# Performance work log

Hardware: AMD Instinct MI355X
Metric: run time of the kernel (lower is better)

## Reference

```python
import jax, jax.numpy as jnp
import numpy as np

N, C, B, HF, WF, HID = 200000, 128, 4, 116, 200, 64
STRIDE = 8
MAX_BEV_RANGE = 72.0
LN_EPS = 1e-5


def setup_inputs() -> dict:
    key = jax.random.key(0)
    ks = jax.random.split(key, 20)
    s = 0.05  # weight scale
    x = jax.random.normal(ks[0], (N, C), jnp.float32)
    # sparse voxel indices: (batch, z, y, x) on a 128x128x5 stride-8 grid
    bi = jax.random.randint(ks[1], (N, 1), 0, B)
    zi = jax.random.randint(ks[2], (N, 1), 0, 5)
    yi = jax.random.randint(ks[3], (N, 1), 0, 128)
    xi = jax.random.randint(ks[4], (N, 1), 0, 128)
    indices = jnp.concatenate([bi, zi, yi, xi], axis=1).astype(jnp.int32)
    voxel_size = jnp.array([0.1, 0.1, 0.2], jnp.float32)
    pc_range = jnp.array([-51.2, -51.2, -5.0, 51.2, 51.2, 3.0], jnp.float32)
    # plausible lidar->image projection: cam_x=-y, cam_y=-z, cam_z=x, K=[1000,800;1000,450]
    Rt = np.array([[0.0, -1.0, 0.0, 0.0],
                   [0.0, 0.0, -1.0, 1.6],
                   [1.0, 0.0, 0.0, 0.0]], np.float32)
    K = np.array([[1000.0, 0.0, 800.0], [0.0, 1000.0, 450.0], [0.0, 0.0, 1.0]], np.float32)
    P = K @ Rt  # [3,4]
    trans = jnp.asarray(np.tile(P[None], (B, 1, 1)))
    trans = trans + 0.01 * jax.random.normal(ks[5], (B, 3, 4), jnp.float32)
    img_feats = jax.random.normal(ks[6], (B, C, HF, WF), jnp.float32)
    return {
        'x': x, 'indices': indices, 'voxel_size': voxel_size, 'pc_range': pc_range,
        'trans_lidar_to_img': trans, 'img_feats': img_feats, 'img_h': 928, 'img_w': 1600,
        'fg_w1': s * jax.random.normal(ks[7], (C, HID)), 'fg_b1': jnp.zeros((HID,)),
        'fg_w2': s * jax.random.normal(ks[8], (HID, 1)), 'fg_b2': jnp.zeros((1,)),
        'rt_w1': s * jax.random.normal(ks[9], (C + 3, HID)), 'rt_b1': jnp.zeros((HID,)),
        'rt_w2': s * jax.random.normal(ks[10], (HID, 3)),
        'rt_b2': jnp.array([2.0, 0.0, -1.0], jnp.float32),
        'le_w1': s * jax.random.normal(ks[11], (2 * C, C)), 'le_b1': jnp.zeros((C,)),
        'le_w2': s * jax.random.normal(ks[12], (C, C)), 'le_b2': jnp.zeros((C,)),
        'ln_g': jnp.ones((C,)), 'ln_b': jnp.zeros((C,)),
    }


def _bilinear_sample(img_t, b, u_norm, v_norm):
    # img_t: [B,H,W,C]; grid_sample bilinear, align_corners=True, padding_mode='zeros'
    Hf, Wf = img_t.shape[1], img_t.shape[2]
    px = (u_norm + 1.0) * 0.5 * (Wf - 1)
    py = (v_norm + 1.0) * 0.5 * (Hf - 1)
    x0 = jnp.floor(px)
    y0 = jnp.floor(py)
    fx, fy = px - x0, py - y0
    x0i, y0i = x0.astype(jnp.int32), y0.astype(jnp.int32)
    out = jnp.zeros((px.shape[0], img_t.shape[-1]), img_t.dtype)
    for dy in (0, 1):
        for dx in (0, 1):
            xi, yi = x0i + dx, y0i + dy
            w = (fx if dx else 1.0 - fx) * (fy if dy else 1.0 - fy)
            inb = (xi >= 0) & (xi < Wf) & (yi >= 0) & (yi < Hf)
            f = img_t[b, jnp.clip(yi, 0, Hf - 1), jnp.clip(xi, 0, Wf - 1)]
            out = out + f * (w * inb.astype(w.dtype))[:, None]
    return out


def _layernorm(h, g, b):
    mu = jnp.mean(h, axis=-1, keepdims=True)
    var = jnp.mean(jnp.square(h - mu), axis=-1, keepdims=True)
    return (h - mu) * jax.lax.rsqrt(var + LN_EPS) * g + b


def reference(x, indices, voxel_size, pc_range, trans_lidar_to_img, img_feats,
              img_h, img_w, fg_w1, fg_b1, fg_w2, fg_b2, rt_w1, rt_b1, rt_w2, rt_b2,
              le_w1, le_b1, le_w2, le_b2, ln_g, ln_b):
    # voxel centers: indices[:,1:]=(z,y,x) -> (x,y,z)
    spatial = indices[:, 1:][:, ::-1].astype(jnp.float32)
    cvs = voxel_size * STRIDE
    centers = spatial * cvs + pc_range[:3] + cvs / 2.0  # [N,3]
    range_norm = jnp.linalg.norm(centers[:, :2], axis=-1, keepdims=True)
    range_norm = jnp.clip(range_norm / max(MAX_BEV_RANGE, 1e-6), 0.0, 1.0)

    # project to image plane
    ones = jnp.ones((centers.shape[0], 1), centers.dtype)
    xyz_hom = jnp.concatenate([centers, ones], axis=1)  # [N,4]
    batch_ids = indices[:, 0]
    P = trans_lidar_to_img[batch_ids]  # [N,3,4]
    pts = jnp.einsum('nij,nj->ni', P, xyz_hom)
    depth = pts[:, 2]
    safe = jnp.maximum(depth, 1e-5)
    u_feat = pts[:, 0] / safe * (float(WF) / float(img_w))
    v_feat = pts[:, 1] / safe * (float(HF) / float(img_h))
    u_norm = 2.0 * (u_feat / max(WF - 1, 1)) - 1.0
    v_norm = 2.0 * (v_feat / max(HF - 1, 1)) - 1.0
    valid = (depth > 1e-5) & (jnp.abs(u_norm) <= 1.0) & (jnp.abs(v_norm) <= 1.0)
    valid_f = valid.astype(jnp.float32)[:, None]  # [N,1]

    # router
    p_fg = jax.nn.sigmoid(jax.nn.relu(x @ fg_w1 + fg_b1) @ fg_w2 + fg_b2)  # [N,1]
    rin = jnp.concatenate([x, range_norm, p_fg, valid_f], axis=-1)
    route_weights = jax.nn.softmax(jax.nn.relu(rin @ rt_w1 + rt_b1) @ rt_w2 + rt_b2, axis=-1)

    # per-point grid_sample gather from image features
    img_t = jnp.transpose(img_feats, (0, 2, 3, 1))  # [B,H,W,C]
    sampled = _bilinear_sample(img_t, batch_ids, u_norm, v_norm)  # [N,C]

    # light fusion expert
    h = jnp.concatenate([x, sampled], axis=-1)
    delta_light = (jax.nn.relu(h @ le_w1 + le_b1) @ le_w2 + le_b2) * valid_f
    delta = route_weights[:, 1:2] * delta_light  # rectified expert disabled (RECTIFY_RATIO=0)

    fusion_gain = jnp.linalg.norm(delta, axis=-1, keepdims=True) / (
        jnp.linalg.norm(x, axis=-1, keepdims=True) + 1e-6)
    fusion_gain = jnp.clip(1.0 - jnp.exp(-fusion_gain), 0.0, 1.0)

    fused = _layernorm(x + delta, ln_g, ln_b)  # [N,C]

    zeros1 = jnp.zeros_like(p_fg)
    quality = jnp.clip(jnp.concatenate(
        [route_weights, p_fg, range_norm, valid_f, zeros1, fusion_gain,
         zeros1, zeros1, zeros1], axis=-1), 0.0, 1.0)  # [N,11]
    return fused, quality
```

## Files before the change

kernel.cpp:

```cpp
#include <hip/hip_runtime.h>

namespace {

typedef __attribute__((ext_vector_type(8))) short bf16x8;
typedef __attribute__((ext_vector_type(4))) float f32x4;

constexpr int C     = 128;
constexpr int HF    = 116;
constexpr int WF    = 200;
constexpr int PTILE = 32;
constexpr int BLK   = 256;
constexpr int NPTS  = 200000;
constexpr int AS_STRIDE  = 264;
constexpr int HID_STRIDE = 136;

constexpr int W_LE1 = 0;
constexpr int W_LE2 = 32768;
constexpr int W_FG  = 49152;
constexpr int W_RT  = 57344;
constexpr size_t IMG_BYTE_OFF = 131072;

constexpr int IMG_BLOCKS = 4 * HF * 2;
constexpr int WP_BLOCKS  = 256;

__device__ __forceinline__ float b2f(unsigned short u) {
  union { unsigned int i; float f; } v; v.i = ((unsigned int)u) << 16; return v.f;
}
__device__ __forceinline__ unsigned short f2b(float f) {
  union { float f; unsigned int i; } v; v.f = f;
  unsigned int i = v.i;
  return (unsigned short)((i + 0x7fffu + ((i >> 16) & 1u)) >> 16);
}
__device__ __forceinline__ void unp(unsigned int u, float& lo, float& hi) {
  union { unsigned int i; float f; } a, b;
  a.i = u << 16; b.i = u & 0xffff0000u; lo = a.f; hi = b.f;
}
__device__ __forceinline__ unsigned int packb(float a, float b) {
  unsigned int r;
  asm("v_cvt_pk_bf16_f32 %0, %1, %2" : "=v"(r) : "v"(a), "v"(b));
  return r;
}

__global__ __launch_bounds__(BLK) void prep_kernel(
    const float* __restrict__ imgf,
    const float* __restrict__ le_w1, const float* __restrict__ le_w2,
    const float* __restrict__ fg_w1, const float* __restrict__ rt_w1,
    short* __restrict__ wpack, short* __restrict__ imgT) {
  __shared__ short buf[100 * HID_STRIDE];
  const int blk = blockIdx.x;
  if (blk < IMG_BLOCKS) {
    const int half = blk & 1, by = blk >> 1;
    const int b = by / HF, y = by - b * HF;
    const int x0 = half * 100;
    const float* s = imgf + (size_t)b * C * HF * WF + (size_t)y * WF + x0;
    for (int i = threadIdx.x; i < C * 25; i += BLK) {
      int c = i / 25, qx = i - c * 25;
      float4 v = *(const float4*)(s + (size_t)c * (HF * WF) + qx * 4);
      int xb = qx * 4;
      buf[(xb + 0) * HID_STRIDE + c] = (short)f2b(v.x);
      buf[(xb + 1) * HID_STRIDE + c] = (short)f2b(v.y);
      buf[(xb + 2) * HID_STRIDE + c] = (short)f2b(v.z);
      buf[(xb + 3) * HID_STRIDE + c] = (short)f2b(v.w);
    }
    __syncthreads();
    short* d = imgT + ((size_t)(b * HF + y) * WF + x0) * C;
    for (int i = threadIdx.x; i < 100 * 16; i += BLK) {
      int xx = i >> 4, c8 = (i & 15) << 3;
      *(uint4*)(d + (size_t)xx * C + c8) = *(const uint4*)&buf[xx * HID_STRIDE + c8];
    }
  } else {
    int idx = (blk - IMG_BLOCKS) * BLK + threadIdx.x;
    if (idx < 32768) {
      int k = idx >> 7, n = idx & 127;
      wpack[W_LE1 + (((k >> 3) * 128 + n) << 3) + (k & 7)] = (short)f2b(le_w1[idx]);
    } else if (idx < 49152) {
      int l = idx - 32768; int k = l >> 7, n = l & 127;
      wpack[W_LE2 + (((k >> 3) * 128 + n) << 3) + (k & 7)] = (short)f2b(le_w2[l]);
    } else if (idx < 57344) {
      int l = idx - 49152; int k = l >> 6, n = l & 63;
      wpack[W_FG + (((k >> 3) * 64 + n) << 3) + (k & 7)] = (short)f2b(fg_w1[l]);
    } else {
      int l = idx - 57344; int k = l >> 6, n = l & 63;
      wpack[W_RT + (((k >> 3) * 64 + n) << 3) + (k & 7)] = (short)f2b(rt_w1[k * 64 + n]);
    }
  }
}

__global__ __launch_bounds__(BLK, 6) void fuse_kernel(
    const float* __restrict__ x,
    const int*   __restrict__ indices,
    const float* __restrict__ vox, const float* __restrict__ pcr,
    const float* __restrict__ trans,
    const int* __restrict__ imgh_p, const int* __restrict__ imgw_p,
    const float* __restrict__ fg_b1v, const float* __restrict__ fg_w2v,
    const float* __restrict__ fg_b2v,
    const float* __restrict__ rt_w1f,
    const float* __restrict__ rt_b1v, const float* __restrict__ rt_w2v,
    const float* __restrict__ rt_b2v,
    const float* __restrict__ le_b1v, const float* __restrict__ le_b2v,
    const float* __restrict__ ln_gv, const float* __restrict__ ln_bv,
    const short* __restrict__ wpack,
    const short* __restrict__ imgT,
    float* __restrict__ out_fused, float* __restrict__ out_qual) {
  __shared__ short As[PTILE * AS_STRIDE];
  __shared__ float s_rn[32], s_pfg[32], s_valid[32], s_px[32], s_py[32];
  __shared__ float s_gain[32], s_rv[32];
  __shared__ float s_route[32][3];
  __shared__ int   s_bat[32];
  __shared__ __align__(16) float s_lnpart[4][16][4];

  const int tid  = threadIdx.x;
  const int n0   = blockIdx.x * PTILE;
  const int wave = tid >> 6;
  const int lane = tid & 63;
  const int q    = lane >> 4;
  const int nn   = lane & 15;

  {
    const float4* xsrc = (const float4*)(x + (size_t)n0 * C);
    for (int i = tid; i < PTILE * C / 4; i += BLK) {
      float4 v = xsrc[i];
      int p = i >> 5, c4 = (i & 31) * 4;
      uint2 sv = { packb(v.x, v.y), packb(v.z, v.w) };
      *(uint2*)&As[p * AS_STRIDE + c4] = sv;
    }
  }
  if (tid < PTILE) {
    int p = tid;
    int base = (n0 + p) * 4;
    int bi = indices[base + 0], zi = indices[base + 1];
    int yi = indices[base + 2], xi = indices[base + 3];
    float sp[3] = { (float)xi, (float)yi, (float)zi };
    float cen[3];
#pragma unroll
    for (int k = 0; k < 3; ++k) {
      float cvs = vox[k] * 8.0f;
      cen[k] = sp[k] * cvs + pcr[k] + cvs * 0.5f;
    }
    float rn = sqrtf(cen[0] * cen[0] + cen[1] * cen[1]) / 72.0f;
    rn = fminf(fmaxf(rn, 0.0f), 1.0f);
    float pt[3];
#pragma unroll
    for (int r = 0; r < 3; ++r) {
      const float* row = trans + (bi * 3 + r) * 4;
      pt[r] = row[0] * cen[0] + row[1] * cen[1] + row[2] * cen[2] + row[3];
    }
    float depth = pt[2];
    float safe  = fmaxf(depth, 1e-5f);
    float uf = pt[0] / safe * ((float)WF / (float)imgw_p[0]);
    float vf = pt[1] / safe * ((float)HF / (float)imgh_p[0]);
    float un = 2.0f * (uf / (float)(WF - 1)) - 1.0f;
    float vn = 2.0f * (vf / (float)(HF - 1)) - 1.0f;
    bool valid = (depth > 1e-5f) && (fabsf(un) <= 1.0f) && (fabsf(vn) <= 1.0f);
    s_rn[p] = rn;
    s_valid[p] = valid ? 1.0f : 0.0f;
    s_bat[p] = bi;
    s_px[p] = (un + 1.0f) * 0.5f * (float)(WF - 1);
    s_py[p] = (vn + 1.0f) * 0.5f * (float)(HF - 1);
  }
  __syncthreads();

  f32x4 accS[4];
#pragma unroll
  for (int t = 0; t < 4; ++t) accS[t] = (f32x4){0.f, 0.f, 0.f, 0.f};
  if (wave < 2) {
    const int p0 = wave * 16;
    const bf16x8* Bfg = (const bf16x8*)(wpack + W_FG);
#pragma unroll 2
    for (int ks = 0; ks < 4; ++ks) {
      bf16x8 a = *(const bf16x8*)&As[(p0 + nn) * AS_STRIDE + ks * 32 + q * 8];
#pragma unroll
      for (int t = 0; t < 4; ++t) {
        bf16x8 b = Bfg[(ks * 4 + q) * 64 + t * 16 + nn];
        accS[t] = __builtin_amdgcn_mfma_f32_16x16x32_bf16(a, b, accS[t], 0, 0, 0);
      }
    }
    float part[4] = {0.f, 0.f, 0.f, 0.f};
#pragma unroll
    for (int t = 0; t < 4; ++t) {
      int col = t * 16 + nn;
      float bias = fg_b1v[col];
      float wv2  = fg_w2v[col];
#pragma unroll
      for (int r = 0; r < 4; ++r)
        part[r] += fmaxf(accS[t][r] + bias, 0.f) * wv2;
    }
#pragma unroll
    for (int off = 1; off < 16; off <<= 1) {
#pragma unroll
      for (int r = 0; r < 4; ++r) part[r] += __shfl_xor(part[r], off);
    }
    if (nn == 0) {
      float b2 = fg_b2v[0];
#pragma unroll
      for (int r = 0; r < 4; ++r)
        s_pfg[p0 + q * 4 + r] = 1.f / (1.f + expf(-(part[r] + b2)));
    }
  } else {
    const int p0 = (wave - 2) * 16;
    const bf16x8* Brt = (const bf16x8*)(wpack + W_RT);
#pragma unroll 2
    for (int ks = 0; ks < 4; ++ks) {
      bf16x8 a = *(const bf16x8*)&As[(p0 + nn) * AS_STRIDE + ks * 32 + q * 8];
#pragma unroll
      for (int t = 0; t < 4; ++t) {
        bf16x8 b = Brt[(ks * 4 + q) * 64 + t * 16 + nn];
        accS[t] = __builtin_amdgcn_mfma_f32_16x16x32_bf16(a, b, accS[t], 0, 0, 0);
      }
    }
  }
  __syncthreads();

  if (wave >= 2) {
    const int p0 = (wave - 2) * 16;
    float lg0[4] = {0,0,0,0}, lg1[4] = {0,0,0,0}, lg2[4] = {0,0,0,0};
#pragma unroll
    for (int t = 0; t < 4; ++t) {
      int col = t * 16 + nn;
      float b1 = rt_b1v[col];
      float wr = rt_w1f[128 * 64 + col];
      float wp = rt_w1f[129 * 64 + col];
      float wv = rt_w1f[130 * 64 + col];
      float w20 = rt_w2v[col * 3 + 0], w21 = rt_w2v[col * 3 + 1], w22 = rt_w2v[col * 3 + 2];
#pragma unroll
      for (int r = 0; r < 4; ++r) {
        int p = p0 + q * 4 + r;
        float h = accS[t][r] + b1 + s_rn[p] * wr + s_pfg[p] * wp + s_valid[p] * wv;
        h = fmaxf(h, 0.f);
        lg0[r] += h * w20; lg1[r] += h * w21; lg2[r] += h * w22;
      }
    }
#pragma unroll
    for (int off = 1; off < 16; off <<= 1) {
#pragma unroll
      for (int r = 0; r < 4; ++r) {
        lg0[r] += __shfl_xor(lg0[r], off);
        lg1[r] += __shfl_xor(lg1[r], off);
        lg2[r] += __shfl_xor(lg2[r], off);
      }
    }
    if (nn == 0) {
      float rb0 = rt_b2v[0], rb1 = rt_b2v[1], rb2 = rt_b2v[2];
#pragma unroll
      for (int r = 0; r < 4; ++r) {
        int p = p0 + q * 4 + r;
        float l0 = lg0[r] + rb0, l1 = lg1[r] + rb1, l2 = lg2[r] + rb2;
        float m = fmaxf(l0, fmaxf(l1, l2));
        float e0 = expf(l0 - m), e1 = expf(l1 - m), e2 = expf(l2 - m);
        float inv = 1.f / (e0 + e1 + e2);
        s_route[p][0] = e0 * inv; s_route[p][1] = e1 * inv; s_route[p][2] = e2 * inv;
        s_rv[p] = e1 * inv * s_valid[p];
      }
    }
  }
  {
    int p = tid >> 3, grp = tid & 7, ch0 = grp * 16;
    float sacc[16];
#pragma unroll
    for (int k = 0; k < 16; ++k) sacc[k] = 0.f;
    if (s_valid[p] > 0.5f) {
      float px = s_px[p], py = s_py[p];
      float x0f = floorf(px), y0f = floorf(py);
      float fx = px - x0f, fy = py - y0f;
      int ix = (int)x0f, iy = (int)y0f;
      int bb = s_bat[p];
#pragma unroll
      for (int dy = 0; dy < 2; ++dy) {
#pragma unroll
        for (int dx = 0; dx < 2; ++dx) {
          int xi = ix + dx, yi = iy + dy;
          if (xi >= 0 && xi < WF && yi >= 0 && yi < HF) {
            float w = (dx ? fx : 1.0f - fx) * (dy ? fy : 1.0f - fy);
            const short* tp = imgT + (((size_t)bb * HF + yi) * WF + xi) * C + ch0;
            uint4 u0 = *(const uint4*)tp;
            uint4 u1 = *(const uint4*)(tp + 8);
            float lo, hi;
            unp(u0.x, lo, hi); sacc[0] += w * lo;  sacc[1] += w * hi;
            unp(u0.y, lo, hi); sacc[2] += w * lo;  sacc[3] += w * hi;
            unp(u0.z, lo, hi); sacc[4] += w * lo;  sacc[5] += w * hi;
            unp(u0.w, lo, hi); sacc[6] += w * lo;  sacc[7] += w * hi;
            unp(u1.x, lo, hi); sacc[8] += w * lo;  sacc[9] += w * hi;
            unp(u1.y, lo, hi); sacc[10] += w * lo; sacc[11] += w * hi;
            unp(u1.z, lo, hi); sacc[12] += w * lo; sacc[13] += w * hi;
            unp(u1.w, lo, hi); sacc[14] += w * lo; sacc[15] += w * hi;
          }
        }
      }
    }
    uint4 o0 = { packb(sacc[0], sacc[1]),  packb(sacc[2], sacc[3]),
                 packb(sacc[4], sacc[5]),  packb(sacc[6], sacc[7]) };
    uint4 o1 = { packb(sacc[8], sacc[9]),  packb(sacc[10], sacc[11]),
                 packb(sacc[12], sacc[13]), packb(sacc[14], sacc[15]) };
    *(uint4*)&As[p * AS_STRIDE + 128 + ch0]     = o0;
    *(uint4*)&As[p * AS_STRIDE + 128 + ch0 + 8] = o1;
  }
  __syncthreads();

  const int pt = wave & 1, cg = wave >> 1;
  const int p0le = pt * 16;
  const bf16x8* Ble1 = (const bf16x8*)(wpack + W_LE1);
  f32x4 acc[4];
#pragma unroll
  for (int t = 0; t < 4; ++t) acc[t] = (f32x4){0.f, 0.f, 0.f, 0.f};
#pragma unroll 2
  for (int ks = 0; ks < 8; ++ks) {
    bf16x8 a = *(const bf16x8*)&As[(p0le + nn) * AS_STRIDE + ks * 32 + q * 8];
#pragma unroll
    for (int t = 0; t < 4; ++t) {
      bf16x8 b = Ble1[(ks * 4 + q) * 128 + (cg * 4 + t) * 16 + nn];
      acc[t] = __builtin_amdgcn_mfma_f32_16x16x32_bf16(a, b, acc[t], 0, 0, 0);
    }
  }
  __syncthreads();
#pragma unroll
  for (int t = 0; t < 4; ++t) {
    int col = (cg * 4 + t) * 16 + nn;
    float bias = le_b1v[col];
#pragma unroll
    for (int r = 0; r < 4; ++r)
      As[(p0le + q * 4 + r) * AS_STRIDE + 128 + col] =
          (short)f2b(fmaxf(acc[t][r] + bias, 0.f));
  }
  __syncthreads();

  const bf16x8* Ble2 = (const bf16x8*)(wpack + W_LE2);
  f32x4 acc2[4];
#pragma unroll
  for (int t = 0; t < 4; ++t) acc2[t] = (f32x4){0.f, 0.f, 0.f, 0.f};
#pragma unroll 2
  for (int ks = 0; ks < 4; ++ks) {
    bf16x8 a = *(const bf16x8*)&As[(p0le + nn) * AS_STRIDE + 128 + ks * 32 + q * 8];
#pragma unroll
    for (int t = 0; t < 4; ++t) {
      bf16x8 b = Ble2[(ks * 4 + q) * 128 + (cg * 4 + t) * 16 + nn];
      acc2[t] = __builtin_amdgcn_mfma_f32_16x16x32_bf16(a, b, acc2[t], 0, 0, 0);
    }
  }
  float yv[4][4];
  float psum[4] = {0,0,0,0}, psum2[4] = {0,0,0,0}, pd2[4] = {0,0,0,0}, px2[4] = {0,0,0,0};
#pragma unroll
  for (int t = 0; t < 4; ++t) {
    int col = (cg * 4 + t) * 16 + nn;
    float bias = le_b2v[col];
#pragma unroll
    for (int r = 0; r < 4; ++r) {
      int p = p0le + q * 4 + r;
      float d  = (acc2[t][r] + bias) * s_rv[p];
      float xv = b2f((unsigned short)As[p * AS_STRIDE + col]);
      float y  = xv + d;
      yv[t][r] = y;
      psum[r]  += y;       psum2[r] += y * y;
      pd2[r]   += d * d;   px2[r]   += xv * xv;
    }
  }
#pragma unroll
  for (int off = 1; off < 16; off <<= 1) {
#pragma unroll
    for (int r = 0; r < 4; ++r) {
      psum[r]  += __shfl_xor(psum[r], off);
      psum2[r] += __shfl_xor(psum2[r], off);
      pd2[r]   += __shfl_xor(pd2[r], off);
      px2[r]   += __shfl_xor(px2[r], off);
    }
  }
  if (nn == 0) {
#pragma unroll
    for (int r = 0; r < 4; ++r) {
      f32x4 st = { psum[r], psum2[r], pd2[r], px2[r] };
      *(f32x4*)&s_lnpart[wave][q * 4 + r][0] = st;
    }
  }
  __syncthreads();
  {
    float gcol[4], bcol[4];
#pragma unroll
    for (int t = 0; t < 4; ++t) {
      int col = (cg * 4 + t) * 16 + nn;
      gcol[t] = ln_gv[col]; bcol[t] = ln_bv[col];
    }
#pragma unroll
    for (int r = 0; r < 4; ++r) {
      int lr = q * 4 + r;
      int p  = p0le + lr;
      f32x4 oth = *(const f32x4*)&s_lnpart[wave ^ 2][lr][0];
      float sy  = psum[r]  + oth[0];
      float sy2 = psum2[r] + oth[1];
      float sd2 = pd2[r]   + oth[2];
      float sx2 = px2[r]   + oth[3];
      float mu  = sy * (1.f / 128.f);
      float var = sy2 * (1.f / 128.f) - mu * mu;
      float inv = rsqrtf(var + 1e-5f);
      if (wave < 2 && nn == 0) {
        float gain = sqrtf(sd2) / (sqrtf(sx2) + 1e-6f);
        s_gain[p] = fminf(fmaxf(1.f - expf(-gain), 0.f), 1.f);
      }
      float* orow = out_fused + (size_t)(n0 + p) * C;
#pragma unroll
      for (int t = 0; t < 4; ++t) {
        int col = (cg * 4 + t) * 16 + nn;
        orow[col] = (yv[t][r] - mu) * inv * gcol[t] + bcol[t];
      }
    }
  }
  __syncthreads();

  for (int idx = tid; idx < PTILE * 11; idx += BLK) {
    int p2 = idx / 11, k = idx - p2 * 11;
    float v = 0.0f;
    if (k < 3)       v = s_route[p2][k];
    else if (k == 3) v = s_pfg[p2];
    else if (k == 4) v = s_rn[p2];
    else if (k == 5) v = s_valid[p2];
    else if (k == 7) v = s_gain[p2];
    v = fminf(fmaxf(v, 0.0f), 1.0f);
    out_qual[(size_t)(n0 + p2) * 11 + k] = v;
  }
}

}

extern "C" void kernel_launch(void* const* d_in, const int* in_sizes, int n_in,
                              void* d_out, int out_size, void* d_ws, size_t ws_size,
                              hipStream_t stream) {
  const float* x       = (const float*)d_in[0];
  const int*   indices = (const int*)d_in[1];
  const float* vox     = (const float*)d_in[2];
  const float* pcr     = (const float*)d_in[3];
  const float* trans   = (const float*)d_in[4];
  const float* imgf    = (const float*)d_in[5];
  const int*   imgh    = (const int*)d_in[6];
  const int*   imgw    = (const int*)d_in[7];
  const float* fg_w1   = (const float*)d_in[8];
  const float* fg_b1   = (const float*)d_in[9];
  const float* fg_w2   = (const float*)d_in[10];
  const float* fg_b2   = (const float*)d_in[11];
  const float* rt_w1   = (const float*)d_in[12];
  const float* rt_b1   = (const float*)d_in[13];
  const float* rt_w2   = (const float*)d_in[14];
  const float* rt_b2   = (const float*)d_in[15];
  const float* le_w1   = (const float*)d_in[16];
  const float* le_b1   = (const float*)d_in[17];
  const float* le_w2   = (const float*)d_in[18];
  const float* le_b2   = (const float*)d_in[19];
  const float* ln_g    = (const float*)d_in[20];
  const float* ln_b    = (const float*)d_in[21];

  short* wpack = (short*)d_ws;
  short* imgT  = (short*)((char*)d_ws + IMG_BYTE_OFF);

  float* out_fused = (float*)d_out;
  float* out_qual  = out_fused + (size_t)NPTS * C;

  (void)in_sizes; (void)n_in; (void)out_size; (void)ws_size;

  prep_kernel<<<IMG_BLOCKS + WP_BLOCKS, BLK, 0, stream>>>(
      imgf, le_w1, le_w2, fg_w1, rt_w1, wpack, imgT);
  fuse_kernel<<<NPTS / PTILE, BLK, 0, stream>>>(
      x, indices, vox, pcr, trans, imgh, imgw,
      fg_b1, fg_w2, fg_b2,
      rt_w1, rt_b1, rt_w2, rt_b2,
      le_b1, le_b2, ln_g, ln_b,
      wpack, imgT, out_fused, out_qual);
}
```

Before: 339.7 us.

## Double point tile to 64 and reuse weight fragments across row groups

Raises the per-block point tile from 32 to 64 and restructures the small MLP and light-expert GEMMs so each wave loads B weight fragments once and applies them to several 16-row groups. The first light-expert layer is repartitioned so each wave owns two output column tiles across all 64 rows, and the second layer plus layernorm loop runs over two halves. This is meant to cut redundant global weight loads per point and halve the block count, at the cost of more registers and LDS per block (launch bound lowered to 4 blocks per CU) and extra barriers in the second-layer loop.

```diff
diff --git a/kernel.cpp b/kernel.cpp
--- a/kernel.cpp
+++ b/kernel.cpp
@@ -8,7 +8,7 @@
 constexpr int C     = 128;
 constexpr int HF    = 116;
 constexpr int WF    = 200;
-constexpr int PTILE = 32;
+constexpr int PTILE = 64;
 constexpr int BLK   = 256;
 constexpr int NPTS  = 200000;
 constexpr int AS_STRIDE  = 264;
@@ -86,7 +86,7 @@
   }
 }
 
-__global__ __launch_bounds__(BLK, 6) void fuse_kernel(
+__global__ __launch_bounds__(BLK, 4) void fuse_kernel(
     const float* __restrict__ x,
     const int*   __restrict__ indices,
     const float* __restrict__ vox, const float* __restrict__ pcr,
@@ -103,10 +103,10 @@
     const short* __restrict__ imgT,
     float* __restrict__ out_fused, float* __restrict__ out_qual) {
   __shared__ short As[PTILE * AS_STRIDE];
-  __shared__ float s_rn[32], s_pfg[32], s_valid[32], s_px[32], s_py[32];
-  __shared__ float s_gain[32], s_rv[32];
-  __shared__ float s_route[32][3];
-  __shared__ int   s_bat[32];
+  __shared__ float s_rn[64], s_pfg[64], s_valid[64], s_px[64], s_py[64];
+  __shared__ float s_gain[64], s_rv[64];
+  __shared__ float s_route[64][3];
+  __shared__ int   s_bat[64];
   __shared__ __align__(16) float s_lnpart[4][16][4];
 
   const int tid  = threadIdx.x;
@@ -139,16 +139,16 @@
     }
     float rn = sqrtf(cen[0] * cen[0] + cen[1] * cen[1]) / 72.0f;
     rn = fminf(fmaxf(rn, 0.0f), 1.0f);
-    float pt[3];
+    float pt3[3];
 #pragma unroll
     for (int r = 0; r < 3; ++r) {
       const float* row = trans + (bi * 3 + r) * 4;
-      pt[r] = row[0] * cen[0] + row[1] * cen[1] + row[2] * cen[2] + row[3];
-    }
-    float depth = pt[2];
+      pt3[r] = row[0] * cen[0] + row[1] * cen[1] + row[2] * cen[2] + row[3];
+    }
+    float depth = pt3[2];
     float safe  = fmaxf(depth, 1e-5f);
-    float uf = pt[0] / safe * ((float)WF / (float)imgw_p[0]);
-    float vf = pt[1] / safe * ((float)HF / (float)imgh_p[0]);
+    float uf = pt3[0] / safe * ((float)WF / (float)imgw_p[0]);
+    float vf = pt3[1] / safe * ((float)HF / (float)imgh_p[0]);
     float un = 2.0f * (uf / (float)(WF - 1)) - 1.0f;
     float vn = 2.0f * (vf / (float)(HF - 1)) - 1.0f;
     bool valid = (depth > 1e-5f) && (fabsf(un) <= 1.0f) && (fabsf(vn) <= 1.0f);
@@ -160,60 +160,64 @@
   }
   __syncthreads();
 
-  f32x4 accS[4];
-#pragma unroll
-  for (int t = 0; t < 4; ++t) accS[t] = (f32x4){0.f, 0.f, 0.f, 0.f};
+  const int p032 = (wave & 1) * 32;
+  f32x4 accS[4][2];
+#pragma unroll
+  for (int t = 0; t < 4; ++t)
+#pragma unroll
+    for (int rg = 0; rg < 2; ++rg) accS[t][rg] = (f32x4){0.f, 0.f, 0.f, 0.f};
+  {
+    const bf16x8* Bw = (const bf16x8*)(wpack + (wave < 2 ? W_FG : W_RT));
+    for (int ks = 0; ks < 4; ++ks) {
+      bf16x8 b0 = Bw[(ks * 4 + q) * 64 + 0 * 16 + nn];
+      bf16x8 b1 = Bw[(ks * 4 + q) * 64 + 1 * 16 + nn];
+      bf16x8 b2 = Bw[(ks * 4 + q) * 64 + 2 * 16 + nn];
+      bf16x8 b3 = Bw[(ks * 4 + q) * 64 + 3 * 16 + nn];
+#pragma unroll
+      for (int rg = 0; rg < 2; ++rg) {
+        bf16x8 a = *(const bf16x8*)&As[(p032 + rg * 16 + nn) * AS_STRIDE + ks * 32 + q * 8];
+        accS[0][rg] = __builtin_amdgcn_mfma_f32_16x16x32_bf16(a, b0, accS[0][rg], 0, 0, 0);
+        accS[1][rg] = __builtin_amdgcn_mfma_f32_16x16x32_bf16(a, b1, accS[1][rg], 0, 0, 0);
+        accS[2][rg] = __builtin_amdgcn_mfma_f32_16x16x32_bf16(a, b2, accS[2][rg], 0, 0, 0);
+        accS[3][rg] = __builtin_amdgcn_mfma_f32_16x16x32_bf16(a, b3, accS[3][rg], 0, 0, 0);
+      }
+    }
+  }
   if (wave < 2) {
-    const int p0 = wave * 16;
-    const bf16x8* Bfg = (const bf16x8*)(wpack + W_FG);
-#pragma unroll 2
-    for (int ks = 0; ks < 4; ++ks) {
-      bf16x8 a = *(const bf16x8*)&As[(p0 + nn) * AS_STRIDE + ks * 32 + q * 8];
-#pragma unroll
-      for (int t = 0; t < 4; ++t) {
-        bf16x8 b = Bfg[(ks * 4 + q) * 64 + t * 16 + nn];
-        accS[t] = __builtin_amdgcn_mfma_f32_16x16x32_bf16(a, b, accS[t], 0, 0, 0);
-      }
-    }
-    float part[4] = {0.f, 0.f, 0.f, 0.f};
+    float part[2][4] = {{0.f,0.f,0.f,0.f},{0.f,0.f,0.f,0.f}};
 #pragma unroll
     for (int t = 0; t < 4; ++t) {
       int col = t * 16 + nn;
       float bias = fg_b1v[col];
       float wv2  = fg_w2v[col];
 #pragma unroll
-      for (int r = 0; r < 4; ++r)
-        part[r] += fmaxf(accS[t][r] + bias, 0.f) * wv2;
+      for (int rg = 0; rg < 2; ++rg)
+#pragma unroll
+        for (int r = 0; r < 4; ++r)
+          part[rg][r] += fmaxf(accS[t][rg][r] + bias, 0.f) * wv2;
     }
 #pragma unroll
     for (int off = 1; off < 16; off <<= 1) {
 #pragma unroll
-      for (int r = 0; r < 4; ++r) part[r] += __shfl_xor(part[r], off);
+      for (int rg = 0; rg < 2; ++rg)
+#pragma unroll
+        for (int r = 0; r < 4; ++r) part[rg][r] += __shfl_xor(part[rg][r], off);
     }
     if (nn == 0) {
-      float b2 = fg_b2v[0];
-#pragma unroll
-      for (int r = 0; r < 4; ++r)
-        s_pfg[p0 + q * 4 + r] = 1.f / (1.f + expf(-(part[r] + b2)));
-    }
-  } else {
-    const int p0 = (wave - 2) * 16;
-    const bf16x8* Brt = (const bf16x8*)(wpack + W_RT);
-#pragma unroll 2
-    for (int ks = 0; ks < 4; ++ks) {
-      bf16x8 a = *(const bf16x8*)&As[(p0 + nn) * AS_STRIDE + ks * 32 + q * 8];
-#pragma unroll
-      for (int t = 0; t < 4; ++t) {
-        bf16x8 b = Brt[(ks * 4 + q) * 64 + t * 16 + nn];
-        accS[t] = __builtin_amdgcn_mfma_f32_16x16x32_bf16(a, b, accS[t], 0, 0, 0);
-      }
+      float b2s = fg_b2v[0];
+#pragma unroll
+      for (int rg = 0; rg < 2; ++rg)
+#pragma unroll
+        for (int r = 0; r < 4; ++r)
+          s_pfg[p032 + rg * 16 + q * 4 + r] = 1.f / (1.f + expf(-(part[rg][r] + b2s)));
     }
   }
   __syncthreads();
 
   if (wave >= 2) {
-    const int p0 = (wave - 2) * 16;
-    float lg0[4] = {0,0,0,0}, lg1[4] = {0,0,0,0}, lg2[4] = {0,0,0,0};
+    float lg0[2][4] = {{0,0,0,0},{0,0,0,0}};
+    float lg1[2][4] = {{0,0,0,0},{0,0,0,0}};
+    float lg2[2][4] = {{0,0,0,0},{0,0,0,0}};
 #pragma unroll
     for (int t = 0; t < 4; ++t) {
       int col = t * 16 + nn;
@@ -223,38 +227,44 @@
       float wv = rt_w1f[130 * 64 + col];
       float w20 = rt_w2v[col * 3 + 0], w21 = rt_w2v[col * 3 + 1], w22 = rt_w2v[col * 3 + 2];
 #pragma unroll
-      for (int r = 0; r < 4; ++r) {
-        int p = p0 + q * 4 + r;
-        float h = accS[t][r] + b1 + s_rn[p] * wr + s_pfg[p] * wp + s_valid[p] * wv;
-        h = fmaxf(h, 0.f);
-        lg0[r] += h * w20; lg1[r] += h * w21; lg2[r] += h * w22;
-      }
+      for (int rg = 0; rg < 2; ++rg)
+#pragma unroll
+        for (int r = 0; r < 4; ++r) {
+          int p = p032 + rg * 16 + q * 4 + r;
+          float h = accS[t][rg][r] + b1 + s_rn[p] * wr + s_pfg[p] * wp + s_valid[p] * wv;
+          h = fmaxf(h, 0.f);
+          lg0[rg][r] += h * w20; lg1[rg][r] += h * w21; lg2[rg][r] += h * w22;
+        }
     }
 #pragma unroll
     for (int off = 1; off < 16; off <<= 1) {
 #pragma unroll
-      for (int r = 0; r < 4; ++r) {
-        lg0[r] += __shfl_xor(lg0[r], off);
-        lg1[r] += __shfl_xor(lg1[r], off);
-        lg2[r] += __shfl_xor(lg2[r], off);
-      }
+      for (int rg = 0; rg < 2; ++rg)
+#pragma unroll
+        for (int r = 0; r < 4; ++r) {
+          lg0[rg][r] += __shfl_xor(lg0[rg][r], off);
+          lg1[rg][r] += __shfl_xor(lg1[rg][r], off);
+          lg2[rg][r] += __shfl_xor(lg2[rg][r], off);
+        }
     }
     if (nn == 0) {
       float rb0 = rt_b2v[0], rb1 = rt_b2v[1], rb2 = rt_b2v[2];
 #pragma unroll
-      for (int r = 0; r < 4; ++r) {
-        int p = p0 + q * 4 + r;
-        float l0 = lg0[r] + rb0, l1 = lg1[r] + rb1, l2 = lg2[r] + rb2;
-        float m = fmaxf(l0, fmaxf(l1, l2));
-        float e0 = expf(l0 - m), e1 = expf(l1 - m), e2 = expf(l2 - m);
-        float inv = 1.f / (e0 + e1 + e2);
-        s_route[p][0] = e0 * inv; s_route[p][1] = e1 * inv; s_route[p][2] = e2 * inv;
-        s_rv[p] = e1 * inv * s_valid[p];
-      }
-    }
-  }
-  {
-    int p = tid >> 3, grp = tid & 7, ch0 = grp * 16;
+      for (int rg = 0; rg < 2; ++rg)
+#pragma unroll
+        for (int r = 0; r < 4; ++r) {
+          int p = p032 + rg * 16 + q * 4 + r;
+          float l0 = lg0[rg][r] + rb0, l1 = lg1[rg][r] + rb1, l2 = lg2[rg][r] + rb2;
+          float m = fmaxf(l0, fmaxf(l1, l2));
+          float e0 = expf(l0 - m), e1 = expf(l1 - m), e2 = expf(l2 - m);
+          float inv = 1.f / (e0 + e1 + e2);
+          s_route[p][0] = e0 * inv; s_route[p][1] = e1 * inv; s_route[p][2] = e2 * inv;
+          s_rv[p] = e1 * inv * s_valid[p];
+        }
+    }
+  }
+  for (int it = 0; it < 2; ++it) {
+    int p = it * 32 + (tid >> 3), grp = tid & 7, ch0 = grp * 16;
     float sacc[16];
 #pragma unroll
     for (int k = 0; k < 16; ++k) sacc[k] = 0.f;
@@ -296,113 +306,121 @@
   }
   __syncthreads();
 
+  {
+    const bf16x8* Ble1 = (const bf16x8*)(wpack + W_LE1);
+    f32x4 acc[2][4];
+#pragma unroll
+    for (int t2 = 0; t2 < 2; ++t2)
+#pragma unroll
+      for (int rg = 0; rg < 4; ++rg) acc[t2][rg] = (f32x4){0.f, 0.f, 0.f, 0.f};
+    for (int ks = 0; ks < 8; ++ks) {
+      bf16x8 b0 = Ble1[(ks * 4 + q) * 128 + (wave * 2 + 0) * 16 + nn];
+      bf16x8 b1 = Ble1[(ks * 4 + q) * 128 + (wave * 2 + 1) * 16 + nn];
+#pragma unroll
+      for (int rg = 0; rg < 4; ++rg) {
+        bf16x8 a = *(const bf16x8*)&As[(rg * 16 + nn) * AS_STRIDE + ks * 32 + q * 8];
+        acc[0][rg] = __builtin_amdgcn_mfma_f32_16x16x32_bf16(a, b0, acc[0][rg], 0, 0, 0);
+        acc[1][rg] = __builtin_amdgcn_mfma_f32_16x16x32_bf16(a, b1, acc[1][rg], 0, 0, 0);
+      }
+    }
+    __syncthreads();
+#pragma unroll
+    for (int t2 = 0; t2 < 2; ++t2) {
+      int col = (wave * 2 + t2) * 16 + nn;
+      float bias = le_b1v[col];
+#pragma unroll
+      for (int rg = 0; rg < 4; ++rg)
+#pragma unroll
+        for (int r = 0; r < 4; ++r)
+          As[(rg * 16 + q * 4 + r) * AS_STRIDE + 128 + col] =
+              (short)f2b(fmaxf(acc[t2][rg][r] + bias, 0.f));
+    }
+    __syncthreads();
+  }
+
+  const bf16x8* Ble2 = (const bf16x8*)(wpack + W_LE2);
   const int pt = wave & 1, cg = wave >> 1;
-  const int p0le = pt * 16;
-  const bf16x8* Ble1 = (const bf16x8*)(wpack + W_LE1);
-  f32x4 acc[4];
-#pragma unroll
-  for (int t = 0; t < 4; ++t) acc[t] = (f32x4){0.f, 0.f, 0.f, 0.f};
-#pragma unroll 2
-  for (int ks = 0; ks < 8; ++ks) {
-    bf16x8 a = *(const bf16x8*)&As[(p0le + nn) * AS_STRIDE + ks * 32 + q * 8];
-#pragma unroll
-    for (int t = 0; t < 4; ++t) {
-      bf16x8 b = Ble1[(ks * 4 + q) * 128 + (cg * 4 + t) * 16 + nn];
-      acc[t] = __builtin_amdgcn_mfma_f32_16x16x32_bf16(a, b, acc[t], 0, 0, 0);
-    }
-  }
-  __syncthreads();
-#pragma unroll
-  for (int t = 0; t < 4; ++t) {
-    int col = (cg * 4 + t) * 16 + nn;
-    float bias = le_b1v[col];
-#pragma unroll
-    for (int r = 0; r < 4; ++r)
-      As[(p0le + q * 4 + r) * AS_STRIDE + 128 + col] =
-          (short)f2b(fmaxf(acc[t][r] + bias, 0.f));
-  }
-  __syncthreads();
-
-  const bf16x8* Ble2 = (const bf16x8*)(wpack + W_LE2);
-  f32x4 acc2[4];
-#pragma unroll
-  for (int t = 0; t < 4; ++t) acc2[t] = (f32x4){0.f, 0.f, 0.f, 0.f};
-#pragma unroll 2
-  for (int ks = 0; ks < 4; ++ks) {
-    bf16x8 a = *(const bf16x8*)&As[(p0le + nn) * AS_STRIDE + 128 + ks * 32 + q * 8];
-#pragma unroll
-    for (int t = 0; t < 4; ++t) {
-      bf16x8 b = Ble2[(ks * 4 + q) * 128 + (cg * 4 + t) * 16 + nn];
-      acc2[t] = __builtin_amdgcn_mfma_f32_16x16x32_bf16(a, b, acc2[t], 0, 0, 0);
-    }
-  }
-  float yv[4][4];
-  float psum[4] = {0,0,0,0}, psum2[4] = {0,0,0,0}, pd2[4] = {0,0,0,0}, px2[4] = {0,0,0,0};
-#pragma unroll
-  for (int t = 0; t < 4; ++t) {
-    int col = (cg * 4 + t) * 16 + nn;
-    float bias = le_b2v[col];
-#pragma unroll
-    for (int r = 0; r < 4; ++r) {
-      int p = p0le + q * 4 + r;
-      float d  = (acc2[t][r] + bias) * s_rv[p];
-      float xv = b2f((unsigned short)As[p * AS_STRIDE + col]);
-      float y  = xv + d;
-      yv[t][r] = y;
-      psum[r]  += y;       psum2[r] += y * y;
-      pd2[r]   += d * d;   px2[r]   += xv * xv;
-    }
-  }
-#pragma unroll
-  for (int off = 1; off < 16; off <<= 1) {
-#pragma unroll
-    for (int r = 0; r < 4; ++r) {
-      psum[r]  += __shfl_xor(psum[r], off);
-      psum2[r] += __shfl_xor(psum2[r], off);
-      pd2[r]   += __shfl_xor(pd2[r], off);
-      px2[r]   += __shfl_xor(px2[r], off);
-    }
-  }
-  if (nn == 0) {
-#pragma unroll
-    for (int r = 0; r < 4; ++r) {
-      f32x4 st = { psum[r], psum2[r], pd2[r], px2[r] };
-      *(f32x4*)&s_lnpart[wave][q * 4 + r][0] = st;
-    }
-  }
-  __syncthreads();
-  {
-    float gcol[4], bcol[4];
+  for (int hh = 0; hh < 2; ++hh) {
+    const int p0le = hh * 32 + pt * 16;
+    f32x4 acc2[4];
+#pragma unroll
+    for (int t = 0; t < 4; ++t) acc2[t] = (f32x4){0.f, 0.f, 0.f, 0.f};
+    for (int ks = 0; ks < 4; ++ks) {
+      bf16x8 a = *(const bf16x8*)&As[(p0le + nn) * AS_STRIDE + 128 + ks * 32 + q * 8];
+#pragma unroll
+      for (int t = 0; t < 4; ++t) {
+        bf16x8 b = Ble2[(ks * 4 + q) * 128 + (cg * 4 + t) * 16 + nn];
+        acc2[t] = __builtin_amdgcn_mfma_f32_16x16x32_bf16(a, b, acc2[t], 0, 0, 0);
+      }
+    }
+    float yv[4][4];
+    float psum[4] = {0,0,0,0}, psum2[4] = {0,0,0,0}, pd2[4] = {0,0,0,0}, px2[4] = {0,0,0,0};
 #pragma unroll
     for (int t = 0; t < 4; ++t) {
       int col = (cg * 4 + t) * 16 + nn;
-      gcol[t] = ln_gv[col]; bcol[t] = ln_bv[col];
-    }
-#pragma unroll
-    for (int r = 0; r < 4; ++r) {
-      int lr = q * 4 + r;
-      int p  = p0le + lr;
-      f32x4 oth = *(const f32x4*)&s_lnpart[wave ^ 2][lr][0];
-      float sy  = psum[r]  + oth[0];
-      float sy2 = psum2[r] + oth[1];
-      float sd2 = pd2[r]   + oth[2];
-      float sx2 = px2[r]   + oth[3];
-      float mu  = sy * (1.f / 128.f);
-      float var = sy2 * (1.f / 128.f) - mu * mu;
-      float inv = rsqrtf(var + 1e-5f);
-      if (wave < 2 && nn == 0) {
-        float gain = sqrtf(sd2) / (sqrtf(sx2) + 1e-6f);
-        s_gain[p] = fminf(fmaxf(1.f - expf(-gain), 0.f), 1.f);
-      }
-      float* orow = out_fused + (size_t)(n0 + p) * C;
+      float bias = le_b2v[col];
+#pragma unroll
+      for (int r = 0; r < 4; ++r) {
+        int p = p0le + q * 4 + r;
+        float d  = (acc2[t][r] + bias) * s_rv[p];
+        float xv = b2f((unsigned short)As[p * AS_STRIDE + col]);
+        float y  = xv + d;
+        yv[t][r] = y;
+        psum[r]  += y;       psum2[r] += y * y;
+        pd2[r]   += d * d;   px2[r]   += xv * xv;
+      }
+    }
+#pragma unroll
+    for (int off = 1; off < 16; off <<= 1) {
+#pragma unroll
+      for (int r = 0; r < 4; ++r) {
+        psum[r]  += __shfl_xor(psum[r], off);
+        psum2[r] += __shfl_xor(psum2[r], off);
+        pd2[r]   += __shfl_xor(pd2[r], off);
+        px2[r]   += __shfl_xor(px2[r], off);
+      }
+    }
+    if (nn == 0) {
+#pragma unroll
+      for (int r = 0; r < 4; ++r) {
+        f32x4 st = { psum[r], psum2[r], pd2[r], px2[r] };
+        *(f32x4*)&s_lnpart[wave][q * 4 + r][0] = st;
+      }
+    }
+    __syncthreads();
+    {
+      float gcol[4], bcol[4];
 #pragma unroll
       for (int t = 0; t < 4; ++t) {
         int col = (cg * 4 + t) * 16 + nn;
-        orow[col] = (yv[t][r] - mu) * inv * gcol[t] + bcol[t];
-      }
-    }
-  }
-  __syncthreads();
+        gcol[t] = ln_gv[col]; bcol[t] = ln_bv[col];
+      }
+#pragma unroll
+      for (int r = 0; r < 4; ++r) {
+        int lr = q * 4 + r;
+        int p  = p0le + lr;
+        f32x4 oth = *(const f32x4*)&s_lnpart[wave ^ 2][lr][0];
+        float sy  = psum[r]  + oth[0];
+        float sy2 = psum2[r] + oth[1];
+        float sd2 = pd2[r]   + oth[2];
+        float sx2 = px2[r]   + oth[3];
+        float mu  = sy * (1.f / 128.f);
+        float var = sy2 * (1.f / 128.f) - mu * mu;
+        float inv = rsqrtf(var + 1e-5f);
+        if (wave < 2 && nn == 0) {
+          float gain = sqrtf(sd2) / (sqrtf(sx2) + 1e-6f);
+          s_gain[p] = fminf(fmaxf(1.f - expf(-gain), 0.f), 1.f);
+        }
+        float* orow = out_fused + (size_t)(n0 + p) * C;
+#pragma unroll
+        for (int t = 0; t < 4; ++t) {
+          int col = (cg * 4 + t) * 16 + nn;
+          orow[col] = (yv[t][r] - mu) * inv * gcol[t] + bcol[t];
+        }
+      }
+    }
+    __syncthreads();
+  }
 
   for (int idx = tid; idx < PTILE * 11; idx += BLK) {
     int p2 = idx / 11, k = idx - p2 * 11;
```

Result: slower. 366.2 us (+7.8%).

## Repartition MLP GEMM waves so each loads half the weight columns

Applied to the files above, without the earlier changes.

The light-expert GEMMs switch from a 2x2 split (point half by column half) to giving each of the four waves all 32 points and 32 output columns. Each wave now loads only its two weight column tiles per k-step instead of four, which halves per-wave global weight fetches, while it reads A fragments for both row groups. The LayerNorm partial-sum buffer grows to cover all 32 points, and every wave sums four partials instead of two, adding a little LDS traffic and reduction work.

```diff
diff --git a/kernel.cpp b/kernel.cpp
--- a/kernel.cpp
+++ b/kernel.cpp
@@ -107,7 +107,7 @@
   __shared__ float s_gain[32], s_rv[32];
   __shared__ float s_route[32][3];
   __shared__ int   s_bat[32];
-  __shared__ __align__(16) float s_lnpart[4][16][4];
+  __shared__ __align__(16) float s_lnpart[4][32][4];
 
   const int tid  = threadIdx.x;
   const int n0   = blockIdx.x * PTILE;
@@ -139,16 +139,16 @@
     }
     float rn = sqrtf(cen[0] * cen[0] + cen[1] * cen[1]) / 72.0f;
     rn = fminf(fmaxf(rn, 0.0f), 1.0f);
-    float pt[3];
+    float pt3[3];
 #pragma unroll
     for (int r = 0; r < 3; ++r) {
       const float* row = trans + (bi * 3 + r) * 4;
-      pt[r] = row[0] * cen[0] + row[1] * cen[1] + row[2] * cen[2] + row[3];
-    }
-    float depth = pt[2];
+      pt3[r] = row[0] * cen[0] + row[1] * cen[1] + row[2] * cen[2] + row[3];
+    }
+    float depth = pt3[2];
     float safe  = fmaxf(depth, 1e-5f);
-    float uf = pt[0] / safe * ((float)WF / (float)imgw_p[0]);
-    float vf = pt[1] / safe * ((float)HF / (float)imgh_p[0]);
+    float uf = pt3[0] / safe * ((float)WF / (float)imgw_p[0]);
+    float vf = pt3[1] / safe * ((float)HF / (float)imgh_p[0]);
     float un = 2.0f * (uf / (float)(WF - 1)) - 1.0f;
     float vn = 2.0f * (vf / (float)(HF - 1)) - 1.0f;
     bool valid = (depth > 1e-5f) && (fabsf(un) <= 1.0f) && (fabsf(vn) <= 1.0f);
@@ -296,111 +296,134 @@
   }
   __syncthreads();
 
-  const int pt = wave & 1, cg = wave >> 1;
-  const int p0le = pt * 16;
-  const bf16x8* Ble1 = (const bf16x8*)(wpack + W_LE1);
-  f32x4 acc[4];
-#pragma unroll
-  for (int t = 0; t < 4; ++t) acc[t] = (f32x4){0.f, 0.f, 0.f, 0.f};
+  {
+    const bf16x8* Ble1 = (const bf16x8*)(wpack + W_LE1);
+    f32x4 acc[2][2];
+#pragma unroll
+    for (int rg = 0; rg < 2; ++rg)
+#pragma unroll
+      for (int t2 = 0; t2 < 2; ++t2) acc[rg][t2] = (f32x4){0.f, 0.f, 0.f, 0.f};
 #pragma unroll 2
-  for (int ks = 0; ks < 8; ++ks) {
-    bf16x8 a = *(const bf16x8*)&As[(p0le + nn) * AS_STRIDE + ks * 32 + q * 8];
-#pragma unroll
-    for (int t = 0; t < 4; ++t) {
-      bf16x8 b = Ble1[(ks * 4 + q) * 128 + (cg * 4 + t) * 16 + nn];
-      acc[t] = __builtin_amdgcn_mfma_f32_16x16x32_bf16(a, b, acc[t], 0, 0, 0);
-    }
-  }
-  __syncthreads();
-#pragma unroll
-  for (int t = 0; t < 4; ++t) {
-    int col = (cg * 4 + t) * 16 + nn;
-    float bias = le_b1v[col];
-#pragma unroll
-    for (int r = 0; r < 4; ++r)
-      As[(p0le + q * 4 + r) * AS_STRIDE + 128 + col] =
-          (short)f2b(fmaxf(acc[t][r] + bias, 0.f));
-  }
-  __syncthreads();
+    for (int ks = 0; ks < 8; ++ks) {
+      bf16x8 b0 = Ble1[(ks * 4 + q) * 128 + (wave * 2 + 0) * 16 + nn];
+      bf16x8 b1 = Ble1[(ks * 4 + q) * 128 + (wave * 2 + 1) * 16 + nn];
+#pragma unroll
+      for (int rg = 0; rg < 2; ++rg) {
+        bf16x8 a = *(const bf16x8*)&As[(rg * 16 + nn) * AS_STRIDE + ks * 32 + q * 8];
+        acc[rg][0] = __builtin_amdgcn_mfma_f32_16x16x32_bf16(a, b0, acc[rg][0], 0, 0, 0);
+        acc[rg][1] = __builtin_amdgcn_mfma_f32_16x16x32_bf16(a, b1, acc[rg][1], 0, 0, 0);
+      }
+    }
+    __syncthreads();
+#pragma unroll
+    for (int t2 = 0; t2 < 2; ++t2) {
+      int col = (wave * 2 + t2) * 16 + nn;
+      float bias = le_b1v[col];
+#pragma unroll
+      for (int rg = 0; rg < 2; ++rg)
+#pragma unroll
+        for (int r = 0; r < 4; ++r)
+          As[(rg * 16 + q * 4 + r) * AS_STRIDE + 128 + col] =
+              (short)f2b(fmaxf(acc[rg][t2][r] + bias, 0.f));
+    }
+    __syncthreads();
+  }
 
   const bf16x8* Ble2 = (const bf16x8*)(wpack + W_LE2);
-  f32x4 acc2[4];
-#pragma unroll
-  for (int t = 0; t < 4; ++t) acc2[t] = (f32x4){0.f, 0.f, 0.f, 0.f};
+  f32x4 acc2[2][2];
+#pragma unroll
+  for (int rg = 0; rg < 2; ++rg)
+#pragma unroll
+    for (int t2 = 0; t2 < 2; ++t2) acc2[rg][t2] = (f32x4){0.f, 0.f, 0.f, 0.f};
 #pragma unroll 2
   for (int ks = 0; ks < 4; ++ks) {
-    bf16x8 a = *(const bf16x8*)&As[(p0le + nn) * AS_STRIDE + 128 + ks * 32 + q * 8];
-#pragma unroll
-    for (int t = 0; t < 4; ++t) {
-      bf16x8 b = Ble2[(ks * 4 + q) * 128 + (cg * 4 + t) * 16 + nn];
-      acc2[t] = __builtin_amdgcn_mfma_f32_16x16x32_bf16(a, b, acc2[t], 0, 0, 0);
-    }
-  }
-  float yv[4][4];
-  float psum[4] = {0,0,0,0}, psum2[4] = {0,0,0,0}, pd2[4] = {0,0,0,0}, px2[4] = {0,0,0,0};
-#pragma unroll
-  for (int t = 0; t < 4; ++t) {
-    int col = (cg * 4 + t) * 16 + nn;
+    bf16x8 b0 = Ble2[(ks * 4 + q) * 128 + (wave * 2 + 0) * 16 + nn];
+    bf16x8 b1 = Ble2[(ks * 4 + q) * 128 + (wave * 2 + 1) * 16 + nn];
+#pragma unroll
+    for (int rg = 0; rg < 2; ++rg) {
+      bf16x8 a = *(const bf16x8*)&As[(rg * 16 + nn) * AS_STRIDE + 128 + ks * 32 + q * 8];
+      acc2[rg][0] = __builtin_amdgcn_mfma_f32_16x16x32_bf16(a, b0, acc2[rg][0], 0, 0, 0);
+      acc2[rg][1] = __builtin_amdgcn_mfma_f32_16x16x32_bf16(a, b1, acc2[rg][1], 0, 0, 0);
+    }
+  }
+  float yv[2][2][4];
+  float psum[2][4]  = {{0,0,0,0},{0,0,0,0}};
+  float psum2[2][4] = {{0,0,0,0},{0,0,0,0}};
+  float pd2[2][4]   = {{0,0,0,0},{0,0,0,0}};
+  float px2[2][4]   = {{0,0,0,0},{0,0,0,0}};
+#pragma unroll
+  for (int t2 = 0; t2 < 2; ++t2) {
+    int col = (wave * 2 + t2) * 16 + nn;
     float bias = le_b2v[col];
 #pragma unroll
-    for (int r = 0; r < 4; ++r) {
-      int p = p0le + q * 4 + r;
-      float d  = (acc2[t][r] + bias) * s_rv[p];
-      float xv = b2f((unsigned short)As[p * AS_STRIDE + col]);
-      float y  = xv + d;
-      yv[t][r] = y;
-      psum[r]  += y;       psum2[r] += y * y;
-      pd2[r]   += d * d;   px2[r]   += xv * xv;
-    }
+    for (int rg = 0; rg < 2; ++rg)
+#pragma unroll
+      for (int r = 0; r < 4; ++r) {
+        int p = rg * 16 + q * 4 + r;
+        float d  = (acc2[rg][t2][r] + bias) * s_rv[p];
+        float xv = b2f((unsigned short)As[p * AS_STRIDE + col]);
+        float y  = xv + d;
+        yv[rg][t2][r] = y;
+        psum[rg][r]  += y;       psum2[rg][r] += y * y;
+        pd2[rg][r]   += d * d;   px2[rg][r]   += xv * xv;
+      }
   }
 #pragma unroll
   for (int off = 1; off < 16; off <<= 1) {
 #pragma unroll
-    for (int r = 0; r < 4; ++r) {
-      psum[r]  += __shfl_xor(psum[r], off);
-      psum2[r] += __shfl_xor(psum2[r], off);
-      pd2[r]   += __shfl_xor(pd2[r], off);
-      px2[r]   += __shfl_xor(px2[r], off);
-    }
+    for (int rg = 0; rg < 2; ++rg)
+#pragma unroll
+      for (int r = 0; r < 4; ++r) {
+        psum[rg][r]  += __shfl_xor(psum[rg][r], off);
+        psum2[rg][r] += __shfl_xor(psum2[rg][r], off);
+        pd2[rg][r]   += __shfl_xor(pd2[rg][r], off);
+        px2[rg][r]   += __shfl_xor(px2[rg][r], off);
+      }
   }
   if (nn == 0) {
 #pragma unroll
-    for (int r = 0; r < 4; ++r) {
-      f32x4 st = { psum[r], psum2[r], pd2[r], px2[r] };
-      *(f32x4*)&s_lnpart[wave][q * 4 + r][0] = st;
-    }
+    for (int rg = 0; rg < 2; ++rg)
+#pragma unroll
+      for (int r = 0; r < 4; ++r) {
+        f32x4 st = { psum[rg][r], psum2[rg][r], pd2[rg][r], px2[rg][r] };
+        *(f32x4*)&s_lnpart[wave][rg * 16 + q * 4 + r][0] = st;
+      }
   }
   __syncthreads();
   {
-    float gcol[4], bcol[4];
-#pragma unroll
-    for (int t = 0; t < 4; ++t) {
-      int col = (cg * 4 + t) * 16 + nn;
-      gcol[t] = ln_gv[col]; bcol[t] = ln_bv[col];
-    }
-#pragma unroll
-    for (int r = 0; r < 4; ++r) {
-      int lr = q * 4 + r;
-      int p  = p0le + lr;
-      f32x4 oth = *(const f32x4*)&s_lnpart[wave ^ 2][lr][0];
-      float sy  = psum[r]  + oth[0];
-      float sy2 = psum2[r] + oth[1];
-      float sd2 = pd2[r]   + oth[2];
-      float sx2 = px2[r]   + oth[3];
-      float mu  = sy * (1.f / 128.f);
-      float var = sy2 * (1.f / 128.f) - mu * mu;
-      float inv = rsqrtf(var + 1e-5f);
-      if (wave < 2 && nn == 0) {
-        float gain = sqrtf(sd2) / (sqrtf(sx2) + 1e-6f);
-        s_gain[p] = fminf(fmaxf(1.f - expf(-gain), 0.f), 1.f);
-      }
-      float* orow = out_fused + (size_t)(n0 + p) * C;
-#pragma unroll
-      for (int t = 0; t < 4; ++t) {
-        int col = (cg * 4 + t) * 16 + nn;
-        orow[col] = (yv[t][r] - mu) * inv * gcol[t] + bcol[t];
-      }
-    }
+    float gcol[2], bcol[2];
+#pragma unroll
+    for (int t2 = 0; t2 < 2; ++t2) {
+      int col = (wave * 2 + t2) * 16 + nn;
+      gcol[t2] = ln_gv[col]; bcol[t2] = ln_bv[col];
+    }
+#pragma unroll
+    for (int rg = 0; rg < 2; ++rg)
+#pragma unroll
+      for (int r = 0; r < 4; ++r) {
+        int p = rg * 16 + q * 4 + r;
+        f32x4 s0 = *(const f32x4*)&s_lnpart[0][p][0];
+        f32x4 s1 = *(const f32x4*)&s_lnpart[1][p][0];
+        f32x4 s2 = *(const f32x4*)&s_lnpart[2][p][0];
+        f32x4 s3 = *(const f32x4*)&s_lnpart[3][p][0];
+        float sy  = s0[0] + s1[0] + s2[0] + s3[0];
+        float sy2 = s0[1] + s1[1] + s2[1] + s3[1];
+        float sd2 = s0[2] + s1[2] + s2[2] + s3[2];
+        float sx2 = s0[3] + s1[3] + s2[3] + s3[3];
+        float mu  = sy * (1.f / 128.f);
+        float var = sy2 * (1.f / 128.f) - mu * mu;
+        float inv = rsqrtf(var + 1e-5f);
+        if (wave == 0 && nn == 0) {
+          float gain = sqrtf(sd2) / (sqrtf(sx2) + 1e-6f);
+          s_gain[p] = fminf(fmaxf(1.f - expf(-gain), 0.f), 1.f);
+        }
+        float* orow = out_fused + (size_t)(n0 + p) * C;
+#pragma unroll
+        for (int t2 = 0; t2 < 2; ++t2) {
+          int col = (wave * 2 + t2) * 16 + nn;
+          orow[col] = (yv[rg][t2][r] - mu) * inv * gcol[t2] + bcol[t2];
+        }
+      }
   }
   __syncthreads();
 
```

Result: slower. 372.2 us (+9.6%).
